# Kernel optimization log

Hardware: AMD Instinct MI355X
Metric: run time of the kernel (lower is better)

## Reference

```python
import math
import jax, jax.numpy as jnp
import numpy as np

GROUPS = 8
EPS = 1e-5


def setup_inputs() -> dict:
    key = jax.random.key(0)
    ks = jax.random.split(key, 4)
    B, C, H, W = 4, 128, 64, 64
    x = jax.random.normal(ks[0], (B, C, H, W), dtype=jnp.float32)
    norm_w = jnp.ones((C,), dtype=jnp.float32)
    norm_b = jnp.zeros((C,), dtype=jnp.float32)
    qkv_w = jax.random.normal(ks[1], (3 * C, C), dtype=jnp.float32) * 0.02
    qkv_b = jnp.zeros((3 * C,), dtype=jnp.float32)
    proj_w = jax.random.normal(ks[2], (C, C), dtype=jnp.float32) * 0.02
    proj_b = jnp.zeros((C,), dtype=jnp.float32)
    return {"x": x, "norm_w": norm_w, "norm_b": norm_b,
            "qkv_w": qkv_w, "qkv_b": qkv_b,
            "proj_w": proj_w, "proj_b": proj_b}


def reference(x, norm_w, norm_b, qkv_w, qkv_b, proj_w, proj_b):
    B, C, H, W = x.shape
    N = H * W
    # GroupNorm over (C/G, H, W) per group
    xr = x.reshape(B, GROUPS, C // GROUPS, N)
    mean = xr.mean(axis=(2, 3), keepdims=True)
    var = xr.var(axis=(2, 3), keepdims=True)
    h = ((xr - mean) * jax.lax.rsqrt(var + EPS)).reshape(B, C, N)
    h = h * norm_w[None, :, None] + norm_b[None, :, None]
    # 1x1 conv QKV == per-pixel linear: [B, 3C, N]
    qkv = jnp.einsum('oc,bcn->bon', qkv_w, h) + qkv_b[None, :, None]
    q, k, v = jnp.split(qkv, 3, axis=1)  # each [B, C, N]
    scale = 1.0 / math.sqrt(C)
    attn = jax.nn.softmax(jnp.einsum('bci,bcj->bij', q, k) * scale, axis=-1)  # [B,N,N]
    out = jnp.einsum('bij,bcj->bci', attn, v)  # [B, C, N]
    proj = jnp.einsum('oc,bcn->bon', proj_w, out) + proj_b[None, :, None]
    return x + proj.reshape(B, C, H, W)
```

## Files before the change

### kernel.cpp

```cpp
#include <hip/hip_runtime.h>

typedef float  f32x4   __attribute__((ext_vector_type(4)));
typedef float  f32x16  __attribute__((ext_vector_type(16)));
typedef short  bf16x8  __attribute__((ext_vector_type(8)));
typedef unsigned short u16;

constexpr int B_ = 4;
constexpr int C_ = 128;
constexpr int N_ = 4096;
constexpr int G_ = 8;
constexpr int CperG = 16;
constexpr float EPS_ = 1e-5f;
constexpr float SCALE2_ = 0.08838834764831845f * 1.4426950408889634f;

__device__ inline u16 f2bf(float f) {
    union { float f; unsigned u; } v; v.f = f;
    unsigned r = v.u + 0x7fffu + ((v.u >> 16) & 1u);
    return (u16)(r >> 16);
}
__device__ inline unsigned cvtpk(float lo, float hi) {
    unsigned r;
    asm("v_cvt_pk_bf16_f32 %0, %1, %2" : "=v"(r) : "v"(lo), "v"(hi));
    return r;
}

__global__ __launch_bounds__(256) void prep_kernel(const float* __restrict__ x,
                                                   const float* __restrict__ qw,
                                                   const float* __restrict__ pw,
                                                   float* __restrict__ stats2,
                                                   u16* __restrict__ qwbf,
                                                   u16* __restrict__ pwbf) {
    int blk = blockIdx.x;
    if (blk < 256) {
        __shared__ float rs[4], rss[4];
        int bg = blk >> 3, chunk = blk & 7;
        const float4* xp = (const float4*)(x + (size_t)bg * (CperG * N_)) + chunk * 2048;
        float s = 0.f, ss = 0.f;
        for (int i = threadIdx.x; i < 2048; i += 256) {
            float4 v = xp[i];
            s  += v.x + v.y + v.z + v.w;
            ss += v.x*v.x + v.y*v.y + v.z*v.z + v.w*v.w;
        }
        #pragma unroll
        for (int off = 32; off > 0; off >>= 1) {
            s  += __shfl_down(s, off);
            ss += __shfl_down(ss, off);
        }
        int wv = threadIdx.x >> 6, ln = threadIdx.x & 63;
        if (ln == 0) { rs[wv] = s; rss[wv] = ss; }
        __syncthreads();
        if (threadIdx.x == 0) {
            stats2[blk*2]     = rs[0] + rs[1] + rs[2] + rs[3];
            stats2[blk*2 + 1] = rss[0] + rss[1] + rss[2] + rss[3];
        }
    } else {
        int fidx = ((blk - 256) * 256 + threadIdx.x) * 4;
        float4 v;
        u16* dst;
        if (fidx < 3*C_*C_) { v = *(const float4*)(qw + fidx); dst = qwbf + fidx; }
        else { int j = fidx - 3*C_*C_; v = *(const float4*)(pw + j); dst = pwbf + j; }
        ushort4 o;
        o.x = f2bf(v.x); o.y = f2bf(v.y); o.z = f2bf(v.z); o.w = f2bf(v.w);
        *(ushort4*)dst = o;
    }
}

constexpr int HS = 136;

__global__ __launch_bounds__(256, 3) void qkv_kernel(const float* __restrict__ x,
                                                     const float* __restrict__ stats2,
                                                     const float* __restrict__ nw,
                                                     const float* __restrict__ nb,
                                                     const u16* __restrict__ qwbf,
                                                     const float* __restrict__ qb,
                                                     u16* __restrict__ Qt,
                                                     u16* __restrict__ Ksw,
                                                     u16* __restrict__ Vsw,
                                                     float* __restrict__ qn2,
                                                     int* __restrict__ kmaxI) {
    int blk = blockIdx.x & 255;
    int sec = blockIdx.x >> 8;
    int n0 = (blk & 63) * 64;
    int b  = blk >> 6;
    __shared__ u16 hs[64 * HS];
    __shared__ u16 Wl[64 * HS];
    __shared__ float gmean[8], grstd[8];
    int t = threadIdx.x;
    const float invM = 1.f / (float)(CperG * N_);
    if (t < 8) {
        const float* sp = stats2 + (size_t)(b*G_ + t)*16;
        float S = 0.f, SS = 0.f;
        #pragma unroll
        for (int k2 = 0; k2 < 8; ++k2) { S += sp[k2*2]; SS += sp[k2*2 + 1]; }
        float mean = S * invM;
        gmean[t] = mean;
        grstd[t] = rsqrtf(SS * invM - mean*mean + EPS_);
    }
    __syncthreads();
    #pragma unroll
    for (int r = 0; r < 8; ++r) {
        int idx = t + (r << 8);
        int c = idx >> 4, n4 = idx & 15;
        int g = c >> 4;
        float wgt = nw[c] * grstd[g];
        float bia = nb[c] - gmean[g] * wgt;
        float4 xv = *(const float4*)(x + ((size_t)(b*C_ + c))*N_ + n0 + n4*4);
        int base = (n4*4) * HS + c;
        unsigned u01 = cvtpk(xv.x*wgt + bia, xv.y*wgt + bia);
        unsigned u23 = cvtpk(xv.z*wgt + bia, xv.w*wgt + bia);
        hs[base         ] = (u16)(u01 & 0xffffu);
        hs[base +     HS] = (u16)(u01 >> 16);
        hs[base + 2 * HS] = (u16)(u23 & 0xffffu);
        hs[base + 3 * HS] = (u16)(u23 >> 16);
    }
    __syncthreads();
    int w = t >> 6, lane = t & 63, lo = lane & 15, hi = lane >> 4;
    bf16x8 hf[4];
    #pragma unroll
    for (int ch = 0; ch < 4; ++ch)
        hf[ch] = *(const bf16x8*)(hs + (16*w + lo)*HS + 32*ch + 8*hi);

    int Tb = (n0 >> 5) + (w >> 1);
    float nq = 0.f, nk = 0.f;
    for (int ckj = 0; ckj < 2; ++ckj) {
        int ck = 2*sec + ckj;
        {
            int r = t >> 2, p = t & 3;
            const u16* src = qwbf + (size_t)(ck*64 + r)*C_ + p*32;
            u16* dst = Wl + r*HS + p*32;
            #pragma unroll
            for (int k2 = 0; k2 < 4; ++k2)
                *(uint4*)(dst + 8*k2) = *(const uint4*)(src + 8*k2);
        }
        __syncthreads();
        #pragma unroll
        for (int ot = 0; ot < 4; ++ot) {
            int o16 = ck*64 + ot*16;
            bf16x8 wf[4];
            #pragma unroll
            for (int ch = 0; ch < 4; ++ch)
                wf[ch] = *(const bf16x8*)(Wl + (ot*16 + lo)*HS + 32*ch + 8*hi);
            if (o16 < 2*C_) {
                f32x4 acc = (f32x4){0.f, 0.f, 0.f, 0.f};
                #pragma unroll
                for (int ch = 0; ch < 4; ++ch)
                    acc = __builtin_amdgcn_mfma_f32_16x16x32_bf16(wf[ch], hf[ch], acc, 0, 0, 0);
                float4 bv = *(const float4*)(qb + o16 + 4*hi);
                int n = n0 + 16*w + lo;
                if (o16 < C_) {
                    float q0 = (acc[0] + bv.x) * SCALE2_;
                    float q1 = (acc[1] + bv.y) * SCALE2_;
                    float q2 = (acc[2] + bv.z) * SCALE2_;
                    float q3 = (acc[3] + bv.w) * SCALE2_;
                    nq += (q0*q0 + q1*q1) + (q2*q2 + q3*q3);
                    union { ushort4 s4; unsigned u[2]; } o4;
                    o4.u[0] = cvtpk(q0, q1);
                    o4.u[1] = cvtpk(q2, q3);
                    *(ushort4*)(Qt + ((size_t)b*N_ + n)*C_ + o16 + 4*hi) = o4.s4;
                } else {
                    float k0 = acc[0] + bv.x, k1 = acc[1] + bv.y;
                    float k2 = acc[2] + bv.z, k3 = acc[3] + bv.w;
                    nk += (k0*k0 + k1*k1) + (k2*k2 + k3*k3);
                    union { ushort4 s4; unsigned u[2]; } o4;
                    o4.u[0] = cvtpk(k0, k1);
                    o4.u[1] = cvtpk(k2, k3);
                    int cc = (o16 - C_) >> 4;
                    int lp = (16*(w & 1) + lo) + 32*(hi >> 1);
                    size_t fb = ((size_t)(b*128 + Tb)*8 + cc)*512;
                    *(ushort4*)(Ksw + fb + lp*8 + 4*(hi & 1)) = o4.s4;
                }
            } else {
                f32x4 acc = (f32x4){0.f, 0.f, 0.f, 0.f};
                #pragma unroll
                for (int ch = 0; ch < 4; ++ch)
                    acc = __builtin_amdgcn_mfma_f32_16x16x32_bf16(hf[ch], wf[ch], acc, 0, 0, 0);
                float bia = qb[o16 + lo];
                union { ushort4 s4; unsigned u[2]; } o4;
                o4.u[0] = cvtpk(acc[0] + bia, acc[1] + bia);
                o4.u[1] = cvtpk(acc[2] + bia, acc[3] + bia);
                int m  = (o16 - 2*C_) >> 4;
                int ct = m >> 1;
                int lp = (16*(m & 1) + lo) + 32*(hi & 1);
                size_t fb = (((size_t)(b*4 + ct)*128 + Tb)*2 + (w & 1))*512;
                *(ushort4*)(Vsw + fb + lp*8 + 4*(hi >> 1)) = o4.s4;
            }
        }
        __syncthreads();
    }
    if (sec == 0) {
        nq += __shfl_xor(nq, 16); nq += __shfl_xor(nq, 32);
        if (lane < 16) qn2[(size_t)b*N_ + n0 + 16*w + lo] = nq;
    } else if (sec == 1) {
        nk += __shfl_xor(nk, 16); nk += __shfl_xor(nk, 32);
        #pragma unroll
        for (int off = 1; off < 16; off <<= 1)
            nk = fmaxf(nk, __shfl_xor(nk, off));
        if (lane == 0) atomicMax(&kmaxI[b], __float_as_int(nk));
    }
}

__global__ __launch_bounds__(512, 2) void attn_kernel(const u16* __restrict__ Qt,
                                                      const u16* __restrict__ Ksw,
                                                      const u16* __restrict__ Vsw,
                                                      const float* __restrict__ qn2,
                                                      const int* __restrict__ kmaxI,
                                                      const u16* __restrict__ pwbf,
                                                      const float* __restrict__ pb,
                                                      const float* __restrict__ x,
                                                      float* __restrict__ out) {
    int lb = blockIdx.x;
    int b  = lb & 3;
    int i0 = 64 * (lb >> 2);
    int t = threadIdx.x;
    int w = t >> 6, lane = t & 63;
    int l31 = lane & 31, h = lane >> 5;
    int qt = w >> 2, ks = w & 3;

    __shared__ float Ob[64 * 132];
    __shared__ float lW[8][32];

    float kmax = sqrtf(__int_as_float(kmaxI[b]));
    float mq = sqrtf(qn2[(size_t)b*N_ + i0 + 32*qt + l31]) * kmax * 1.02f + 1e-6f;

    const u16* Qb = Qt + (size_t)b*N_*C_;
    bf16x8 qf[8];
    #pragma unroll
    for (int cc = 0; cc < 8; ++cc)
        qf[cc] = *(const bf16x8*)(Qb + (size_t)(i0 + 32*qt + l31)*C_ + 16*cc + 8*h);

    f32x16 acc[4];
    #pragma unroll
    for (int ct = 0; ct < 4; ++ct)
        #pragma unroll
        for (int r = 0; r < 16; ++r) acc[ct][r] = 0.f;
    float ps0 = 0.f, ps1 = 0.f, ps2 = 0.f, ps3 = 0.f;

    const u16* Kbase = Ksw + ((size_t)(b*128 + ks*32)*8)*512;
    bf16x8 kf[8], kn[8];
    #pragma unroll
    for (int cc = 0; cc < 8; ++cc)
        kf[cc] = *(const bf16x8*)(Kbase + cc*512 + lane*8);
    bf16x8 v1[4], v2[4], w1[4], w2[4];
    #pragma unroll
    for (int ct = 0; ct < 4; ++ct) {
        const u16* vb = Vsw + (((size_t)(b*4 + ct)*128 + ks*32)*2)*512;
        v1[ct] = *(const bf16x8*)(vb + lane*8);
        v2[ct] = *(const bf16x8*)(vb + 512 + lane*8);
    }

    for (int it = 0; it < 32; ++it) {
        f32x16 s;
        #pragma unroll
        for (int r = 0; r < 16; ++r) s[r] = 0.f;
        #pragma unroll
        for (int cc = 0; cc < 8; ++cc)
            s = __builtin_amdgcn_mfma_f32_32x32x16_bf16(kf[cc], qf[cc], s, 0, 0, 0);
        int itn = (it + 1) & 31;
        {
            const u16* Kn = Kbase + ((size_t)itn*8)*512;
            #pragma unroll
            for (int cc = 0; cc < 8; ++cc)
                kn[cc] = *(const bf16x8*)(Kn + cc*512 + lane*8);
        }
        {
            int Tn = ks*32 + itn;
            #pragma unroll
            for (int ct = 0; ct < 4; ++ct) {
                const u16* vb = Vsw + (((size_t)(b*4 + ct)*128 + Tn)*2)*512;
                w1[ct] = *(const bf16x8*)(vb + lane*8);
                w2[ct] = *(const bf16x8*)(vb + 512 + lane*8);
            }
        }
        float p[16];
        #pragma unroll
        for (int r = 0; r < 16; ++r)
            p[r] = __builtin_amdgcn_exp2f(s[r] - mq);
        #pragma unroll
        for (int r = 0; r < 16; r += 4) {
            ps0 += p[r];     ps1 += p[r + 1];
            ps2 += p[r + 2]; ps3 += p[r + 3];
        }
        union { bf16x8 v; unsigned u[4]; } pf1, pf2;
        pf1.u[0] = cvtpk(p[0],  p[1]);  pf1.u[1] = cvtpk(p[2],  p[3]);
        pf1.u[2] = cvtpk(p[4],  p[5]);  pf1.u[3] = cvtpk(p[6],  p[7]);
        pf2.u[0] = cvtpk(p[8],  p[9]);  pf2.u[1] = cvtpk(p[10], p[11]);
        pf2.u[2] = cvtpk(p[12], p[13]); pf2.u[3] = cvtpk(p[14], p[15]);
        #pragma unroll
        for (int ct = 0; ct < 4; ++ct) {
            acc[ct] = __builtin_amdgcn_mfma_f32_32x32x16_bf16(v1[ct], pf1.v, acc[ct], 0, 0, 0);
            acc[ct] = __builtin_amdgcn_mfma_f32_32x32x16_bf16(v2[ct], pf2.v, acc[ct], 0, 0, 0);
        }
        #pragma unroll
        for (int cc = 0; cc < 8; ++cc) kf[cc] = kn[cc];
        #pragma unroll
        for (int ct = 0; ct < 4; ++ct) { v1[ct] = w1[ct]; v2[ct] = w2[ct]; }
    }

    float psum = (ps0 + ps1) + (ps2 + ps3);
    psum += __shfl_xor(psum, 32);
    if (lane < 32) lW[w][l31] = psum;
    for (int i = 0; i < 4; ++i) {
        if (ks == i) {
            int q = 32*qt + l31;
            #pragma unroll
            for (int ct = 0; ct < 4; ++ct)
                #pragma unroll
                for (int qd = 0; qd < 4; ++qd) {
                    int c = 32*ct + 8*qd + 4*h;
                    float4 vv;
                    vv.x = acc[ct][4*qd + 0];
                    vv.y = acc[ct][4*qd + 1];
                    vv.z = acc[ct][4*qd + 2];
                    vv.w = acc[ct][4*qd + 3];
                    if (i == 0) {
                        *(float4*)(Ob + q*132 + c) = vv;
                    } else {
                        float4 o = *(const float4*)(Ob + q*132 + c);
                        o.x += vv.x; o.y += vv.y; o.z += vv.z; o.w += vv.w;
                        *(float4*)(Ob + q*132 + c) = o;
                    }
                }
        }
        __syncthreads();
    }
    int lo = lane & 15, hi = lane >> 4;
    int qtile = w >> 1, os = w & 1;
    int q = 16*qtile + lo;
    int qg = 4*(q >> 5), qc = q & 31;
    float linv = 1.f / (lW[qg][qc] + lW[qg+1][qc] + lW[qg+2][qc] + lW[qg+3][qc]);
    bf16x8 aa[4];
    #pragma unroll
    for (int ch = 0; ch < 4; ++ch) {
        float4 ua = *(const float4*)(Ob + q*132 + 32*ch + 8*hi);
        float4 ub = *(const float4*)(Ob + q*132 + 32*ch + 8*hi + 4);
        union { bf16x8 hh; unsigned u[4]; } pkd;
        pkd.u[0] = cvtpk(ua.x*linv, ua.y*linv);
        pkd.u[1] = cvtpk(ua.z*linv, ua.w*linv);
        pkd.u[2] = cvtpk(ub.x*linv, ub.y*linv);
        pkd.u[3] = cvtpk(ub.z*linv, ub.w*linv);
        aa[ch] = pkd.hh;
    }
    #pragma unroll
    for (int ot = 0; ot < 4; ++ot) {
        int ob = 64*os + 16*ot;
        f32x4 pr = (f32x4){0.f, 0.f, 0.f, 0.f};
        #pragma unroll
        for (int ch = 0; ch < 4; ++ch) {
            bf16x8 bw = *(const bf16x8*)(pwbf + (size_t)(ob + lo)*C_ + 32*ch + 8*hi);
            pr = __builtin_amdgcn_mfma_f32_16x16x32_bf16(aa[ch], bw, pr, 0, 0, 0);
        }
        int o = ob + lo;
        float pbv = pb[o];
        size_t base = ((size_t)(b*C_ + o))*N_ + i0 + 16*qtile + 4*hi;
        float4 xr = *(const float4*)(x + base);
        float4 res;
        res.x = xr.x + pr[0] + pbv;
        res.y = xr.y + pr[1] + pbv;
        res.z = xr.z + pr[2] + pbv;
        res.w = xr.w + pr[3] + pbv;
        *(float4*)(out + base) = res;
    }
}

extern "C" void kernel_launch(void* const* d_in, const int* in_sizes, int n_in,
                              void* d_out, int out_size, void* d_ws, size_t ws_size,
                              hipStream_t stream) {
    const float* x  = (const float*)d_in[0];
    const float* nw = (const float*)d_in[1];
    const float* nb = (const float*)d_in[2];
    const float* qw = (const float*)d_in[3];
    const float* qb = (const float*)d_in[4];
    const float* pw = (const float*)d_in[5];
    const float* pb = (const float*)d_in[6];
    float* out = (float*)d_out;

    char* p = (char*)d_ws;
    float* stats2 = (float*)p;                 p += 2048;
    float* qn2    = (float*)p;                 p += (size_t)B_*N_*4;
    int*   kmaxI  = (int*)p;                   p += 256;
    u16*   qwbf   = (u16*)p;                   p += (size_t)3*C_*C_*2;
    u16*   pwbf   = (u16*)p;                   p += (size_t)C_*C_*2;
    u16*   Qt     = (u16*)p;                   p += (size_t)B_*N_*C_*2;
    u16*   Ksw    = (u16*)p;                   p += (size_t)B_*N_*C_*2;
    u16*   Vsw    = (u16*)p;

    prep_kernel<<<dim3(320), 256, 0, stream>>>(x, qw, pw, stats2, qwbf, pwbf);
    qkv_kernel<<<dim3(768), 256, 0, stream>>>(x, stats2, nw, nb, qwbf, qb,
                                              Qt, Ksw, Vsw, qn2, kmaxI);
    attn_kernel<<<dim3(256), 512, 0, stream>>>(Qt, Ksw, Vsw, qn2, kmaxI,
                                               pwbf, pb, x, out);
}
```

Before: 149.2 us.

## Fuse prep, QKV and attention into one cooperative kernel with grid syncs

Replaces the three launches (stats/weight conversion, QKV projection, attention+proj) with a single cooperative kernel of 256 blocks x 512 threads that separates the stages with grid.sync(). This is meant to remove launch gaps and inter-kernel tail effects. The QKV stage is re-tiled so that one block covers all 3C outputs for 64 pixels using two wave groups. The attention stage is unchanged in structure. The change adds grid-barrier cost and cuts QKV-stage parallelism to 256 blocks, and it falls back to the old three-kernel path if the cooperative launch fails.

```diff
diff --git a/kernel.cpp b/kernel.cpp
--- a/kernel.cpp
+++ b/kernel.cpp
@@ -1,4 +1,7 @@
 #include <hip/hip_runtime.h>
+#include <hip/hip_cooperative_groups.h>
+
+namespace cg = cooperative_groups;
 
 typedef float  f32x4   __attribute__((ext_vector_type(4)));
 typedef float  f32x16  __attribute__((ext_vector_type(16)));
@@ -22,6 +25,341 @@
     unsigned r;
     asm("v_cvt_pk_bf16_f32 %0, %1, %2" : "=v"(r) : "v"(lo), "v"(hi));
     return r;
+}
+
+constexpr int HS = 136;
+
+struct SMb { u16 hs[64*HS]; u16 Wl2[2][64*HS]; float gm[8], gr[8]; };
+struct SMc { float Ob[64*132]; float lW[8][32]; };
+union  SMu { struct { float rs[8], rss[8]; } a; SMb b; SMc c; };
+
+__global__ __launch_bounds__(512, 2) void fused_kernel(
+    const float* __restrict__ x,  const float* __restrict__ nw, const float* __restrict__ nb,
+    const float* __restrict__ qw, const float* __restrict__ qb,
+    const float* __restrict__ pw, const float* __restrict__ pb,
+    float* __restrict__ out,
+    float* __restrict__ stats2, float* __restrict__ qn2, int* __restrict__ kmaxI,
+    u16* __restrict__ qwbf, u16* __restrict__ pwbf,
+    u16* __restrict__ Qt,  u16* __restrict__ Ksw, u16* __restrict__ Vsw)
+{
+    __shared__ SMu sm;
+    cg::grid_group grid = cg::this_grid();
+    int blk = blockIdx.x, t = threadIdx.x;
+
+    {
+        int bg = blk >> 3, chunk = blk & 7;
+        const float4* xp = (const float4*)(x + (size_t)bg * (CperG * N_)) + chunk * 2048;
+        float s = 0.f, ss = 0.f;
+        #pragma unroll
+        for (int i = 0; i < 4; ++i) {
+            float4 v = xp[t + (i << 9)];
+            s  += v.x + v.y + v.z + v.w;
+            ss += v.x*v.x + v.y*v.y + v.z*v.z + v.w*v.w;
+        }
+        #pragma unroll
+        for (int off = 32; off > 0; off >>= 1) {
+            s  += __shfl_down(s, off);
+            ss += __shfl_down(ss, off);
+        }
+        int wv = t >> 6, ln = t & 63;
+        if (ln == 0) { sm.a.rs[wv] = s; sm.a.rss[wv] = ss; }
+        if (t < 64) {
+            int fidx = (blk * 64 + t) * 4;
+            float4 v; u16* dst;
+            if (fidx < 3*C_*C_) { v = *(const float4*)(qw + fidx); dst = qwbf + fidx; }
+            else { int j2 = fidx - 3*C_*C_; v = *(const float4*)(pw + j2); dst = pwbf + j2; }
+            ushort4 o;
+            o.x = f2bf(v.x); o.y = f2bf(v.y); o.z = f2bf(v.z); o.w = f2bf(v.w);
+            *(ushort4*)dst = o;
+        }
+        if (blk == 0 && t >= 128 && t < 132) kmaxI[t - 128] = (int)0x80000000;
+        __syncthreads();
+        if (t == 0) {
+            float S = 0.f, SS = 0.f;
+            #pragma unroll
+            for (int k2 = 0; k2 < 8; ++k2) { S += sm.a.rs[k2]; SS += sm.a.rss[k2]; }
+            stats2[blk*2]     = S;
+            stats2[blk*2 + 1] = SS;
+        }
+    }
+    __threadfence();
+    grid.sync();
+
+    {
+        int n0 = (blk & 63) * 64;
+        int b  = blk >> 6;
+        const float invM = 1.f / (float)(CperG * N_);
+        if (t < 8) {
+            const float* sp = stats2 + (size_t)(b*G_ + t)*16;
+            float S = 0.f, SS = 0.f;
+            #pragma unroll
+            for (int k2 = 0; k2 < 8; ++k2) { S += sp[k2*2]; SS += sp[k2*2 + 1]; }
+            float mean = S * invM;
+            sm.b.gm[t] = mean;
+            sm.b.gr[t] = rsqrtf(SS * invM - mean*mean + EPS_);
+        }
+        __syncthreads();
+        #pragma unroll
+        for (int r = 0; r < 4; ++r) {
+            int idx = t + (r << 9);
+            int c = idx >> 4, n4 = idx & 15;
+            int g = c >> 4;
+            float wgt = nw[c] * sm.b.gr[g];
+            float bia = nb[c] - sm.b.gm[g] * wgt;
+            float4 xv = *(const float4*)(x + ((size_t)(b*C_ + c))*N_ + n0 + n4*4);
+            int base = (n4*4) * HS + c;
+            unsigned u01 = cvtpk(xv.x*wgt + bia, xv.y*wgt + bia);
+            unsigned u23 = cvtpk(xv.z*wgt + bia, xv.w*wgt + bia);
+            sm.b.hs[base         ] = (u16)(u01 & 0xffffu);
+            sm.b.hs[base +     HS] = (u16)(u01 >> 16);
+            sm.b.hs[base + 2 * HS] = (u16)(u23 & 0xffffu);
+            sm.b.hs[base + 3 * HS] = (u16)(u23 >> 16);
+        }
+        __syncthreads();
+        int w = t >> 6, lane = t & 63, lo = lane & 15, hi = lane >> 4;
+        int wl = w & 3, grp = w >> 2;
+        bf16x8 hf[4];
+        #pragma unroll
+        for (int ch = 0; ch < 4; ++ch)
+            hf[ch] = *(const bf16x8*)(sm.b.hs + (16*wl + lo)*HS + 32*ch + 8*hi);
+        int Tb = (n0 >> 5) + (wl >> 1);
+        u16* Wl = sm.b.Wl2[grp];
+        float nq = 0.f, nk = 0.f;
+        for (int j = 0; j < 3; ++j) {
+            int ck = 3*grp + j;
+            {
+                int tl = t & 255;
+                int r = tl >> 2, p = tl & 3;
+                const u16* src = qwbf + (size_t)(ck*64 + r)*C_ + p*32;
+                u16* dst = Wl + r*HS + p*32;
+                #pragma unroll
+                for (int k2 = 0; k2 < 4; ++k2)
+                    *(uint4*)(dst + 8*k2) = *(const uint4*)(src + 8*k2);
+            }
+            __syncthreads();
+            #pragma unroll
+            for (int ot = 0; ot < 4; ++ot) {
+                int o16 = ck*64 + ot*16;
+                bf16x8 wf[4];
+                #pragma unroll
+                for (int ch = 0; ch < 4; ++ch)
+                    wf[ch] = *(const bf16x8*)(Wl + (ot*16 + lo)*HS + 32*ch + 8*hi);
+                if (o16 < 2*C_) {
+                    f32x4 acc = (f32x4){0.f, 0.f, 0.f, 0.f};
+                    #pragma unroll
+                    for (int ch = 0; ch < 4; ++ch)
+                        acc = __builtin_amdgcn_mfma_f32_16x16x32_bf16(wf[ch], hf[ch], acc, 0, 0, 0);
+                    float4 bv = *(const float4*)(qb + o16 + 4*hi);
+                    int n = n0 + 16*wl + lo;
+                    if (o16 < C_) {
+                        float q0 = (acc[0] + bv.x) * SCALE2_;
+                        float q1 = (acc[1] + bv.y) * SCALE2_;
+                        float q2 = (acc[2] + bv.z) * SCALE2_;
+                        float q3 = (acc[3] + bv.w) * SCALE2_;
+                        nq += (q0*q0 + q1*q1) + (q2*q2 + q3*q3);
+                        union { ushort4 s4; unsigned u[2]; } o4;
+                        o4.u[0] = cvtpk(q0, q1);
+                        o4.u[1] = cvtpk(q2, q3);
+                        *(ushort4*)(Qt + ((size_t)b*N_ + n)*C_ + o16 + 4*hi) = o4.s4;
+                    } else {
+                        float k0 = acc[0] + bv.x, k1 = acc[1] + bv.y;
+                        float k2 = acc[2] + bv.z, k3 = acc[3] + bv.w;
+                        nk += (k0*k0 + k1*k1) + (k2*k2 + k3*k3);
+                        union { ushort4 s4; unsigned u[2]; } o4;
+                        o4.u[0] = cvtpk(k0, k1);
+                        o4.u[1] = cvtpk(k2, k3);
+                        int cc = (o16 - C_) >> 4;
+                        int lp = (16*(wl & 1) + lo) + 32*(hi >> 1);
+                        size_t fb = ((size_t)(b*128 + Tb)*8 + cc)*512;
+                        *(ushort4*)(Ksw + fb + lp*8 + 4*(hi & 1)) = o4.s4;
+                    }
+                } else {
+                    f32x4 acc = (f32x4){0.f, 0.f, 0.f, 0.f};
+                    #pragma unroll
+                    for (int ch = 0; ch < 4; ++ch)
+                        acc = __builtin_amdgcn_mfma_f32_16x16x32_bf16(hf[ch], wf[ch], acc, 0, 0, 0);
+                    float bia = qb[o16 + lo];
+                    union { ushort4 s4; unsigned u[2]; } o4;
+                    o4.u[0] = cvtpk(acc[0] + bia, acc[1] + bia);
+                    o4.u[1] = cvtpk(acc[2] + bia, acc[3] + bia);
+                    int m  = (o16 - 2*C_) >> 4;
+                    int ct = m >> 1;
+                    int lp = (16*(m & 1) + lo) + 32*(hi & 1);
+                    size_t fb = (((size_t)(b*4 + ct)*128 + Tb)*2 + (wl & 1))*512;
+                    *(ushort4*)(Vsw + fb + lp*8 + 4*(hi >> 1)) = o4.s4;
+                }
+            }
+            __syncthreads();
+        }
+        if (grp == 0) {
+            nq += __shfl_xor(nq, 16); nq += __shfl_xor(nq, 32);
+            if (lane < 16) qn2[(size_t)b*N_ + n0 + 16*wl + lo] = nq;
+        }
+        float* nkx = (float*)sm.b.hs;
+        nk += __shfl_xor(nk, 16); nk += __shfl_xor(nk, 32);
+        if (grp == 1 && lane < 16) nkx[wl*16 + lo] = nk;
+        __syncthreads();
+        if (grp == 0) {
+            nk += nkx[wl*16 + lo];
+            #pragma unroll
+            for (int off = 1; off < 16; off <<= 1)
+                nk = fmaxf(nk, __shfl_xor(nk, off));
+            if (lane == 0) atomicMax(&kmaxI[b], __float_as_int(nk));
+        }
+    }
+    __threadfence();
+    grid.sync();
+
+    {
+        int lb = blk;
+        int b  = lb & 3;
+        int i0 = 64 * (lb >> 2);
+        int w = t >> 6, lane = t & 63;
+        int l31 = lane & 31, h = lane >> 5;
+        int qt = w >> 2, ks = w & 3;
+
+        float kmax = sqrtf(__int_as_float(kmaxI[b]));
+        float mq = sqrtf(qn2[(size_t)b*N_ + i0 + 32*qt + l31]) * kmax * 1.02f + 1e-6f;
+
+        const u16* Qb = Qt + (size_t)b*N_*C_;
+        bf16x8 qf[8];
+        #pragma unroll
+        for (int cc = 0; cc < 8; ++cc)
+            qf[cc] = *(const bf16x8*)(Qb + (size_t)(i0 + 32*qt + l31)*C_ + 16*cc + 8*h);
+
+        f32x16 acc[4];
+        #pragma unroll
+        for (int ct = 0; ct < 4; ++ct)
+            #pragma unroll
+            for (int r = 0; r < 16; ++r) acc[ct][r] = 0.f;
+        float ps0 = 0.f, ps1 = 0.f, ps2 = 0.f, ps3 = 0.f;
+
+        const u16* Kbase = Ksw + ((size_t)(b*128 + ks*32)*8)*512;
+        bf16x8 kf[8], kn[8];
+        #pragma unroll
+        for (int cc = 0; cc < 8; ++cc)
+            kf[cc] = *(const bf16x8*)(Kbase + cc*512 + lane*8);
+        bf16x8 v1[4], v2[4], w1[4], w2[4];
+        #pragma unroll
+        for (int ct = 0; ct < 4; ++ct) {
+            const u16* vb = Vsw + (((size_t)(b*4 + ct)*128 + ks*32)*2)*512;
+            v1[ct] = *(const bf16x8*)(vb + lane*8);
+            v2[ct] = *(const bf16x8*)(vb + 512 + lane*8);
+        }
+
+        for (int it = 0; it < 32; ++it) {
+            f32x16 s;
+            #pragma unroll
+            for (int r = 0; r < 16; ++r) s[r] = 0.f;
+            #pragma unroll
+            for (int cc = 0; cc < 8; ++cc)
+                s = __builtin_amdgcn_mfma_f32_32x32x16_bf16(kf[cc], qf[cc], s, 0, 0, 0);
+            int itn = (it + 1) & 31;
+            {
+                const u16* Kn = Kbase + ((size_t)itn*8)*512;
+                #pragma unroll
+                for (int cc = 0; cc < 8; ++cc)
+                    kn[cc] = *(const bf16x8*)(Kn + cc*512 + lane*8);
+            }
+            {
+                int Tn = ks*32 + itn;
+                #pragma unroll
+                for (int ct = 0; ct < 4; ++ct) {
+                    const u16* vb = Vsw + (((size_t)(b*4 + ct)*128 + Tn)*2)*512;
+                    w1[ct] = *(const bf16x8*)(vb + lane*8);
+                    w2[ct] = *(const bf16x8*)(vb + 512 + lane*8);
+                }
+            }
+            float p[16];
+            #pragma unroll
+            for (int r = 0; r < 16; ++r)
+                p[r] = __builtin_amdgcn_exp2f(s[r] - mq);
+            #pragma unroll
+            for (int r = 0; r < 16; r += 4) {
+                ps0 += p[r];     ps1 += p[r + 1];
+                ps2 += p[r + 2]; ps3 += p[r + 3];
+            }
+            union { bf16x8 v; unsigned u[4]; } pf1, pf2;
+            pf1.u[0] = cvtpk(p[0],  p[1]);  pf1.u[1] = cvtpk(p[2],  p[3]);
+            pf1.u[2] = cvtpk(p[4],  p[5]);  pf1.u[3] = cvtpk(p[6],  p[7]);
+            pf2.u[0] = cvtpk(p[8],  p[9]);  pf2.u[1] = cvtpk(p[10], p[11]);
+            pf2.u[2] = cvtpk(p[12], p[13]); pf2.u[3] = cvtpk(p[14], p[15]);
+            #pragma unroll
+            for (int ct = 0; ct < 4; ++ct) {
+                acc[ct] = __builtin_amdgcn_mfma_f32_32x32x16_bf16(v1[ct], pf1.v, acc[ct], 0, 0, 0);
+                acc[ct] = __builtin_amdgcn_mfma_f32_32x32x16_bf16(v2[ct], pf2.v, acc[ct], 0, 0, 0);
+            }
+            #pragma unroll
+            for (int cc = 0; cc < 8; ++cc) kf[cc] = kn[cc];
+            #pragma unroll
+            for (int ct = 0; ct < 4; ++ct) { v1[ct] = w1[ct]; v2[ct] = w2[ct]; }
+        }
+
+        float psum = (ps0 + ps1) + (ps2 + ps3);
+        psum += __shfl_xor(psum, 32);
+        if (lane < 32) sm.c.lW[w][l31] = psum;
+        for (int i = 0; i < 4; ++i) {
+            if (ks == i) {
+                int q = 32*qt + l31;
+                #pragma unroll
+                for (int ct = 0; ct < 4; ++ct)
+                    #pragma unroll
+                    for (int qd = 0; qd < 4; ++qd) {
+                        int c = 32*ct + 8*qd + 4*h;
+                        float4 vv;
+                        vv.x = acc[ct][4*qd + 0];
+                        vv.y = acc[ct][4*qd + 1];
+                        vv.z = acc[ct][4*qd + 2];
+                        vv.w = acc[ct][4*qd + 3];
+                        if (i == 0) {
+                            *(float4*)(sm.c.Ob + q*132 + c) = vv;
+                        } else {
+                            float4 o = *(const float4*)(sm.c.Ob + q*132 + c);
+                            o.x += vv.x; o.y += vv.y; o.z += vv.z; o.w += vv.w;
+                            *(float4*)(sm.c.Ob + q*132 + c) = o;
+                        }
+                    }
+            }
+            __syncthreads();
+        }
+        int lo = lane & 15, hi = lane >> 4;
+        int qtile = w >> 1, os = w & 1;
+        int q = 16*qtile + lo;
+        int qg = 4*(q >> 5), qc = q & 31;
+        float linv = 1.f / (sm.c.lW[qg][qc] + sm.c.lW[qg+1][qc] + sm.c.lW[qg+2][qc] + sm.c.lW[qg+3][qc]);
+        bf16x8 aa[4];
+        #pragma unroll
+        for (int ch = 0; ch < 4; ++ch) {
+            float4 ua = *(const float4*)(sm.c.Ob + q*132 + 32*ch + 8*hi);
+            float4 ub = *(const float4*)(sm.c.Ob + q*132 + 32*ch + 8*hi + 4);
+            union { bf16x8 hh; unsigned u[4]; } pkd;
+            pkd.u[0] = cvtpk(ua.x*linv, ua.y*linv);
+            pkd.u[1] = cvtpk(ua.z*linv, ua.w*linv);
+            pkd.u[2] = cvtpk(ub.x*linv, ub.y*linv);
+            pkd.u[3] = cvtpk(ub.z*linv, ub.w*linv);
+            aa[ch] = pkd.hh;
+        }
+        #pragma unroll
+        for (int ot = 0; ot < 4; ++ot) {
+            int ob = 64*os + 16*ot;
+            f32x4 pr = (f32x4){0.f, 0.f, 0.f, 0.f};
+            #pragma unroll
+            for (int ch = 0; ch < 4; ++ch) {
+                bf16x8 bw = *(const bf16x8*)(pwbf + (size_t)(ob + lo)*C_ + 32*ch + 8*hi);
+                pr = __builtin_amdgcn_mfma_f32_16x16x32_bf16(aa[ch], bw, pr, 0, 0, 0);
+            }
+            int o = ob + lo;
+            float pbv = pb[o];
+            size_t base = ((size_t)(b*C_ + o))*N_ + i0 + 16*qtile + 4*hi;
+            float4 xr = *(const float4*)(x + base);
+            float4 res;
+            res.x = xr.x + pr[0] + pbv;
+            res.y = xr.y + pr[1] + pbv;
+            res.z = xr.z + pr[2] + pbv;
+            res.w = xr.w + pr[3] + pbv;
+            *(float4*)(out + base) = res;
+        }
+    }
 }
 
 __global__ __launch_bounds__(256) void prep_kernel(const float* __restrict__ x,
@@ -64,8 +402,6 @@
         *(ushort4*)dst = o;
     }
 }
-
-constexpr int HS = 136;
 
 __global__ __launch_bounds__(256, 3) void qkv_kernel(const float* __restrict__ x,
                                                      const float* __restrict__ stats2,
@@ -384,9 +720,17 @@
     u16*   Ksw    = (u16*)p;                   p += (size_t)B_*N_*C_*2;
     u16*   Vsw    = (u16*)p;
 
-    prep_kernel<<<dim3(320), 256, 0, stream>>>(x, qw, pw, stats2, qwbf, pwbf);
-    qkv_kernel<<<dim3(768), 256, 0, stream>>>(x, stats2, nw, nb, qwbf, qb,
-                                              Qt, Ksw, Vsw, qn2, kmaxI);
-    attn_kernel<<<dim3(256), 512, 0, stream>>>(Qt, Ksw, Vsw, qn2, kmaxI,
-                                               pwbf, pb, x, out);
+    void* args[] = { (void*)&x, (void*)&nw, (void*)&nb, (void*)&qw, (void*)&qb,
+                     (void*)&pw, (void*)&pb, (void*)&out,
+                     (void*)&stats2, (void*)&qn2, (void*)&kmaxI,
+                     (void*)&qwbf, (void*)&pwbf, (void*)&Qt, (void*)&Ksw, (void*)&Vsw };
+    hipError_t err = hipLaunchCooperativeKernel((void*)fused_kernel, dim3(256), dim3(512),
+                                                args, 0, stream);
+    if (err != hipSuccess) {
+        prep_kernel<<<dim3(320), 256, 0, stream>>>(x, qw, pw, stats2, qwbf, pwbf);
+        qkv_kernel<<<dim3(768), 256, 0, stream>>>(x, stats2, nw, nb, qwbf, qb,
+                                                  Qt, Ksw, Vsw, qn2, kmaxI);
+        attn_kernel<<<dim3(256), 512, 0, stream>>>(Qt, Ksw, Vsw, qn2, kmaxI,
+                                                   pwbf, pb, x, out);
+    }
 }
```

Measured after the change: 364.4 us. 2.44x slower.

## Stage K/V tiles through double-buffered LDS with direct global-to-LDS loads

Applied to the files above, without the earlier changes.

Replaces the per-wave register prefetch of K and V fragments with cooperative global_load_lds copies into a double-buffered shared-memory tile, so all eight waves share one load of each K/V chunk instead of the two query-tile waves loading it redundantly. Each iteration issues the next tile's copy, reads fragments from LDS, and synchronises at the end. LDS grows to 128 KB, unioned with the output reduction buffer, and launch bounds drop to one block per CU. This lowers occupancy and adds a block-wide barrier per iteration in exchange for halved global/L2 traffic.

```diff
diff --git a/kernel.cpp b/kernel.cpp
--- a/kernel.cpp
+++ b/kernel.cpp
@@ -4,6 +4,7 @@
 typedef float  f32x16  __attribute__((ext_vector_type(16)));
 typedef short  bf16x8  __attribute__((ext_vector_type(8)));
 typedef unsigned short u16;
+typedef unsigned int   u32;
 
 constexpr int B_ = 4;
 constexpr int C_ = 128;
@@ -22,6 +23,12 @@
     unsigned r;
     asm("v_cvt_pk_bf16_f32 %0, %1, %2" : "=v"(r) : "v"(lo), "v"(hi));
     return r;
+}
+__device__ inline void glds16(const u16* g, u16* l) {
+    __builtin_amdgcn_global_load_lds(
+        (const __attribute__((address_space(1))) u32*)g,
+        (__attribute__((address_space(3))) u32*)l,
+        16, 0, 0);
 }
 
 __global__ __launch_bounds__(256) void prep_kernel(const float* __restrict__ x,
@@ -199,7 +206,7 @@
     }
 }
 
-__global__ __launch_bounds__(512, 2) void attn_kernel(const u16* __restrict__ Qt,
+__global__ __launch_bounds__(512, 1) void attn_kernel(const u16* __restrict__ Qt,
                                                       const u16* __restrict__ Ksw,
                                                       const u16* __restrict__ Vsw,
                                                       const float* __restrict__ qn2,
@@ -216,8 +223,10 @@
     int l31 = lane & 31, h = lane >> 5;
     int qt = w >> 2, ks = w & 3;
 
-    __shared__ float Ob[64 * 132];
-    __shared__ float lW[8][32];
+    __shared__ union {
+        u16 kv[2][32768];
+        struct { float Ob[64*132]; float lW[8][32]; } c;
+    } sm;
 
     float kmax = sqrtf(__int_as_float(kmaxI[b]));
     float mq = sqrtf(qn2[(size_t)b*N_ + i0 + 32*qt + l31]) * kmax * 1.02f + 1e-6f;
@@ -235,41 +244,54 @@
         for (int r = 0; r < 16; ++r) acc[ct][r] = 0.f;
     float ps0 = 0.f, ps1 = 0.f, ps2 = 0.f, ps3 = 0.f;
 
-    const u16* Kbase = Ksw + ((size_t)(b*128 + ks*32)*8)*512;
-    bf16x8 kf[8], kn[8];
-    #pragma unroll
-    for (int cc = 0; cc < 8; ++cc)
-        kf[cc] = *(const bf16x8*)(Kbase + cc*512 + lane*8);
-    bf16x8 v1[4], v2[4], w1[4], w2[4];
-    #pragma unroll
-    for (int ct = 0; ct < 4; ++ct) {
-        const u16* vb = Vsw + (((size_t)(b*4 + ct)*128 + ks*32)*2)*512;
-        v1[ct] = *(const bf16x8*)(vb + lane*8);
-        v2[ct] = *(const bf16x8*)(vb + 512 + lane*8);
-    }
-
-    for (int it = 0; it < 32; ++it) {
+    const u16* gs[8];
+    int loff[8];
+    size_t gstep;
+    if (w < 4) {
+        gstep = 16384;
+        #pragma unroll
+        for (int j = 0; j < 8; ++j) {
+            gs[j]   = Ksw + ((size_t)(b*128 + w)*8 + j)*512 + lane*8;
+            loff[j] = (w*8 + j)*512;
+        }
+    } else {
+        gstep = 4096;
+        int ct = w - 4;
+        #pragma unroll
+        for (int j = 0; j < 8; ++j) {
+            int Tp = j >> 1, kk = j & 1;
+            gs[j]   = Vsw + (((size_t)(b*4 + ct)*128 + Tp)*2 + kk)*512 + lane*8;
+            loff[j] = 16384 + ((ct*4 + Tp)*2 + kk)*512;
+        }
+    }
+
+    #pragma unroll
+    for (int j = 0; j < 8; ++j) { glds16(gs[j], sm.kv[0] + loff[j]); gs[j] += gstep; }
+    __syncthreads();
+
+    for (int tt = 0; tt < 32; ++tt) {
+        if (tt < 31) {
+            u16* dst = sm.kv[(tt + 1) & 1];
+            #pragma unroll
+            for (int j = 0; j < 8; ++j) { glds16(gs[j], dst + loff[j]); gs[j] += gstep; }
+        }
+        const u16* kb = sm.kv[tt & 1];
+        bf16x8 kf[8];
+        #pragma unroll
+        for (int cc = 0; cc < 8; ++cc)
+            kf[cc] = *(const bf16x8*)(kb + (ks*8 + cc)*512 + lane*8);
         f32x16 s;
         #pragma unroll
         for (int r = 0; r < 16; ++r) s[r] = 0.f;
         #pragma unroll
         for (int cc = 0; cc < 8; ++cc)
             s = __builtin_amdgcn_mfma_f32_32x32x16_bf16(kf[cc], qf[cc], s, 0, 0, 0);
-        int itn = (it + 1) & 31;
-        {
-            const u16* Kn = Kbase + ((size_t)itn*8)*512;
-            #pragma unroll
-            for (int cc = 0; cc < 8; ++cc)
-                kn[cc] = *(const bf16x8*)(Kn + cc*512 + lane*8);
-        }
-        {
-            int Tn = ks*32 + itn;
-            #pragma unroll
-            for (int ct = 0; ct < 4; ++ct) {
-                const u16* vb = Vsw + (((size_t)(b*4 + ct)*128 + Tn)*2)*512;
-                w1[ct] = *(const bf16x8*)(vb + lane*8);
-                w2[ct] = *(const bf16x8*)(vb + 512 + lane*8);
-            }
+        bf16x8 v1[4], v2[4];
+        #pragma unroll
+        for (int ct = 0; ct < 4; ++ct) {
+            const u16* vbp = kb + 16384 + ((ct*4 + ks)*2)*512 + lane*8;
+            v1[ct] = *(const bf16x8*)(vbp);
+            v2[ct] = *(const bf16x8*)(vbp + 512);
         }
         float p[16];
         #pragma unroll
@@ -290,15 +312,12 @@
             acc[ct] = __builtin_amdgcn_mfma_f32_32x32x16_bf16(v1[ct], pf1.v, acc[ct], 0, 0, 0);
             acc[ct] = __builtin_amdgcn_mfma_f32_32x32x16_bf16(v2[ct], pf2.v, acc[ct], 0, 0, 0);
         }
-        #pragma unroll
-        for (int cc = 0; cc < 8; ++cc) kf[cc] = kn[cc];
-        #pragma unroll
-        for (int ct = 0; ct < 4; ++ct) { v1[ct] = w1[ct]; v2[ct] = w2[ct]; }
+        __syncthreads();
     }
 
     float psum = (ps0 + ps1) + (ps2 + ps3);
     psum += __shfl_xor(psum, 32);
-    if (lane < 32) lW[w][l31] = psum;
+    if (lane < 32) sm.c.lW[w][l31] = psum;
     for (int i = 0; i < 4; ++i) {
         if (ks == i) {
             int q = 32*qt + l31;
@@ -313,11 +332,11 @@
                     vv.z = acc[ct][4*qd + 2];
                     vv.w = acc[ct][4*qd + 3];
                     if (i == 0) {
-                        *(float4*)(Ob + q*132 + c) = vv;
+                        *(float4*)(sm.c.Ob + q*132 + c) = vv;
                     } else {
-                        float4 o = *(const float4*)(Ob + q*132 + c);
+                        float4 o = *(const float4*)(sm.c.Ob + q*132 + c);
                         o.x += vv.x; o.y += vv.y; o.z += vv.z; o.w += vv.w;
-                        *(float4*)(Ob + q*132 + c) = o;
+                        *(float4*)(sm.c.Ob + q*132 + c) = o;
                     }
                 }
         }
@@ -327,12 +346,12 @@
     int qtile = w >> 1, os = w & 1;
     int q = 16*qtile + lo;
     int qg = 4*(q >> 5), qc = q & 31;
-    float linv = 1.f / (lW[qg][qc] + lW[qg+1][qc] + lW[qg+2][qc] + lW[qg+3][qc]);
+    float linv = 1.f / (sm.c.lW[qg][qc] + sm.c.lW[qg+1][qc] + sm.c.lW[qg+2][qc] + sm.c.lW[qg+3][qc]);
     bf16x8 aa[4];
     #pragma unroll
     for (int ch = 0; ch < 4; ++ch) {
-        float4 ua = *(const float4*)(Ob + q*132 + 32*ch + 8*hi);
-        float4 ub = *(const float4*)(Ob + q*132 + 32*ch + 8*hi + 4);
+        float4 ua = *(const float4*)(sm.c.Ob + q*132 + 32*ch + 8*hi);
+        float4 ub = *(const float4*)(sm.c.Ob + q*132 + 32*ch + 8*hi + 4);
         union { bf16x8 hh; unsigned u[4]; } pkd;
         pkd.u[0] = cvtpk(ua.x*linv, ua.y*linv);
         pkd.u[1] = cvtpk(ua.z*linv, ua.w*linv);
```

After: 147.0 us. Within noise of the previous version (-1.5%).
